# Kernel tuning notes

Hardware: AMD Instinct MI355X
Metric: run time of the kernel (lower is better)

The kernel has to match this reference:

```python
import jax, jax.numpy as jnp
import numpy as np

EMB = 1024
NHEAD = 16
HEAD_DIM = EMB // NHEAD  # 64
L = 2048
NEG = -1e30


def setup_inputs() -> dict:
    key = jax.random.key(0)
    ks = jax.random.split(key, 8)
    # xavier_uniform bound for square [EMB, EMB] matrices
    bound = float(np.sqrt(6.0 / (EMB + EMB)))
    def xavier(k):
        return jax.random.uniform(k, (EMB, EMB), jnp.float32, -bound, bound)
    return {
        "q": jax.random.normal(ks[0], (L, EMB), jnp.float32),
        "k": jax.random.normal(ks[1], (L, EMB), jnp.float32),
        "v": jax.random.normal(ks[2], (L, EMB), jnp.float32),
        "mask": jax.random.randint(ks[3], (NHEAD, L, L), 0, 2) > 0,
        "Wq": xavier(ks[4]),
        "Wk": xavier(ks[5]),
        "Wv": xavier(ks[6]),
        "Wo": xavier(ks[7]),
    }


def reference(q, k, v, mask, Wq, Wk, Wv, Wo):
    scaling = HEAD_DIM ** -0.5
    # F.linear(x, W) = x @ W.T ; reshape to [H, L, D]
    Q = (q @ Wq.T).reshape(L, NHEAD, HEAD_DIM).swapaxes(0, 1)
    K = (k @ Wk.T).reshape(L, NHEAD, HEAD_DIM).swapaxes(0, 1)
    V = (v @ Wv.T).reshape(L, NHEAD, HEAD_DIM).swapaxes(0, 1)
    scores = jnp.einsum("hld,hmd->hlm", Q, K) * scaling  # [H, L, L]
    scores = jnp.where(mask, jnp.asarray(NEG, scores.dtype), scores)
    p = jax.nn.softmax(scores, axis=-1)
    # attn_mask=True: multiplicative re-mask after softmax (custom path)
    p = p * (~mask).astype(p.dtype)
    # dropout is a no-op in eval mode
    attn_out = jnp.einsum("hlm,hmd->hld", p, V)  # [H, L, D]
    attn_out = attn_out.swapaxes(0, 1).reshape(L, EMB)
    return attn_out @ Wo.T
```

## Files before the change

### kernel.cpp

```cpp
#include <hip/hip_runtime.h>
#include <stdint.h>

#define EMB   1024
#define NHEAD 16
#define HDIM  64
#define SEQ   2048

typedef unsigned short ushort_t;
typedef unsigned int   uint32;
typedef __attribute__((ext_vector_type(8))) short bfrag;
typedef __attribute__((ext_vector_type(4))) float ffrag;

#define MFMA(a, b, c) __builtin_amdgcn_mfma_f32_16x16x32_bf16((a), (b), (c), 0, 0, 0)

__device__ inline ushort_t f2bf(float f) {
  uint32 u = __float_as_uint(f);
  u += 0x7FFFu + ((u >> 16) & 1u);
  return (ushort_t)(u >> 16);
}
__device__ inline uint32 pack2(float a, float b) {
  return (uint32)f2bf(a) | ((uint32)f2bf(b) << 16);
}

__device__ inline void glds16(const ushort_t* g, ushort_t* l) {
  __builtin_amdgcn_global_load_lds(
      (const __attribute__((address_space(1))) uint32*)(uintptr_t)g,
      (__attribute__((address_space(3))) uint32*)(uintptr_t)l, 16, 0, 0);
}

__global__ void detect_mask_kernel(const uint32* __restrict__ mw, int* __restrict__ flag) {
  uint32 w = mw[threadIdx.x];
  bool is4 = (w == 0u) || (w == 1u) || (w == 0x3F800000u);
  unsigned long long bad = __ballot(!is4);
  if (threadIdx.x == 0) flag[0] = (bad == 0ull) ? 1 : 0;
}

__global__ __launch_bounds__(256) void compress_mask(
    const void* __restrict__ maskp, const int* __restrict__ flag, ushort_t* __restrict__ bm)
{
  size_t t = (size_t)blockIdx.x * 256 + threadIdx.x;
  size_t row = t >> 7;
  int c16 = (int)(t & 127);
  size_t base = row * SEQ + (size_t)c16 * 16;
  ushort_t mv = 0;
  if (*flag) {
    const uint4* p = (const uint4*)((const uint32*)maskp + base);
    uint4 a0 = p[0], a1 = p[1], a2 = p[2], a3 = p[3];
    uint32 aw[16] = {a0.x,a0.y,a0.z,a0.w, a1.x,a1.y,a1.z,a1.w,
                     a2.x,a2.y,a2.z,a2.w, a3.x,a3.y,a3.z,a3.w};
    #pragma unroll
    for (int i = 0; i < 16; ++i) mv |= (ushort_t)((aw[i] != 0u) ? 1u : 0u) << i;
  } else {
    uint4 b0 = *(const uint4*)((const unsigned char*)maskp + base);
    uint32 bw[4] = {b0.x, b0.y, b0.z, b0.w};
    #pragma unroll
    for (int i = 0; i < 16; ++i)
      mv |= (ushort_t)((((bw[i >> 2] >> ((i & 3) * 8)) & 0xFFu) != 0u) ? 1u : 0u) << i;
  }
  bm[t] = mv;
}

__global__ __launch_bounds__(256) void cvt_all(
    const float4* __restrict__ q,  const float4* __restrict__ k,  const float4* __restrict__ v,
    const float4* __restrict__ wq, const float4* __restrict__ wk, const float4* __restrict__ wv,
    const float4* __restrict__ wo,
    uint2* __restrict__ qb,  uint2* __restrict__ kb,  uint2* __restrict__ vb,
    uint2* __restrict__ wqb, uint2* __restrict__ wkb, uint2* __restrict__ wvb,
    uint2* __restrict__ wob)
{
  int t = blockIdx.x * 256 + threadIdx.x;
  int s = blockIdx.y;
  const float4* src; uint2* dst; int n4;
  switch (s) {
    case 0: src = q;  dst = qb;  n4 = (SEQ * EMB) / 4; break;
    case 1: src = k;  dst = kb;  n4 = (SEQ * EMB) / 4; break;
    case 2: src = v;  dst = vb;  n4 = (SEQ * EMB) / 4; break;
    case 3: src = wq; dst = wqb; n4 = (EMB * EMB) / 4; break;
    case 4: src = wk; dst = wkb; n4 = (EMB * EMB) / 4; break;
    case 5: src = wv; dst = wvb; n4 = (EMB * EMB) / 4; break;
    default: src = wo; dst = wob; n4 = (EMB * EMB) / 4; break;
  }
  if (t >= n4) return;
  float4 f = src[t];
  uint2 o; o.x = pack2(f.x, f.y); o.y = pack2(f.z, f.w);
  dst[t] = o;
}

template<int MODE, int BN>
__device__ inline void gemm_body(const ushort_t* A, const ushort_t* B, void* Cp,
                                 int m0, int n0, ushort_t* As, ushort_t* Bs) {
  const int tid = threadIdx.x, lane = tid & 63, w = tid >> 6;
  const int wm = (w >> 1) * 64, wn = (w & 1) * (BN / 2);
  const int col = lane & 15, g = lane >> 4;
  constexpr int TN = BN / 32;
  constexpr int BIT = BN / 32;

  ffrag acc[4][TN] = {};

  for (int k0 = 0; k0 < EMB; k0 += 64) {
    __syncthreads();
    #pragma unroll
    for (int it = 0; it < 4; ++it) {
      int p = it * 256 + tid;
      int row = p >> 3, pc = p & 7;
      glds16(A + (size_t)(m0 + row) * EMB + k0 + (pc ^ (row & 7)) * 8, &As[p * 8]);
    }
    #pragma unroll
    for (int it = 0; it < BIT; ++it) {
      int p = it * 256 + tid;
      int row = p >> 3, pc = p & 7;
      glds16(B + (size_t)(n0 + row) * EMB + k0 + (pc ^ (row & 7)) * 8, &Bs[p * 8]);
    }
    __syncthreads();

    #pragma unroll
    for (int c = 0; c < 2; ++c) {
      bfrag av[4], bv[TN];
      #pragma unroll
      for (int t = 0; t < 4; ++t) {
        int ra = wm + t * 16 + col;
        av[t] = *(const bfrag*)&As[ra * 64 + ((c * 4 + g) ^ (ra & 7)) * 8];
      }
      #pragma unroll
      for (int t = 0; t < TN; ++t) {
        int rb = wn + t * 16 + col;
        bv[t] = *(const bfrag*)&Bs[rb * 64 + ((c * 4 + g) ^ (rb & 7)) * 8];
      }
      #pragma unroll
      for (int tm = 0; tm < 4; ++tm)
        #pragma unroll
        for (int tn = 0; tn < TN; ++tn)
          acc[tm][tn] = MFMA(av[tm], bv[tn], acc[tm][tn]);
    }
  }

  const int rbase = g * 4;
  #pragma unroll
  for (int tm = 0; tm < 4; ++tm)
    #pragma unroll
    for (int tn = 0; tn < TN; ++tn)
      #pragma unroll
      for (int r = 0; r < 4; ++r) {
        int m = m0 + wm + tm * 16 + rbase + r;
        int n = n0 + wn + tn * 16 + col;
        float vv = acc[tm][tn][r];
        if (MODE == 0) {
          ((ushort_t*)Cp)[((size_t)(n >> 6) * SEQ + m) * HDIM + (n & 63)] = f2bf(vv);
        } else if (MODE == 1) {
          ((ushort_t*)Cp)[((size_t)(m >> 6) * HDIM + (m & 63)) * SEQ + n] = f2bf(vv);
        } else {
          ((float*)Cp)[(size_t)m * EMB + n] = vv;
        }
      }
}

__global__ __launch_bounds__(256) void gemm_qkv(
    const ushort_t* __restrict__ qb, const ushort_t* __restrict__ kb, const ushort_t* __restrict__ vb,
    const ushort_t* __restrict__ Wqb, const ushort_t* __restrict__ Wkb, const ushort_t* __restrict__ Wvb,
    ushort_t* __restrict__ Qb, ushort_t* __restrict__ Kb, ushort_t* __restrict__ Vtb)
{
  __shared__ ushort_t As[128 * 64];
  __shared__ ushort_t Bs[64 * 64];
  const int z = blockIdx.y, bid = blockIdx.x;
  if (z == 0) {
    gemm_body<0, 64>(qb, Wqb, Qb, (bid >> 4) * 128, (bid & 15) * 64, As, Bs);
  } else if (z == 1) {
    gemm_body<0, 64>(kb, Wkb, Kb, (bid >> 4) * 128, (bid & 15) * 64, As, Bs);
  } else {
    gemm_body<1, 64>(Wvb, vb, Vtb, (bid >> 5) * 128, (bid & 31) * 64, As, Bs);
  }
}

__global__ __launch_bounds__(256) void gemm_out(
    const ushort_t* __restrict__ A, const ushort_t* __restrict__ B, float* __restrict__ C)
{
  __shared__ ushort_t As[128 * 64];
  __shared__ ushort_t Bs[64 * 64];
  gemm_body<2, 64>(A, B, (void*)C, blockIdx.y * 128, blockIdx.x * 64, As, Bs);
}

__global__ __launch_bounds__(256) void attn_mfma(
    const ushort_t* __restrict__ Qb,
    const ushort_t* __restrict__ Kb,
    const ushort_t* __restrict__ Vtb,
    const ushort_t* __restrict__ bm,
    ushort_t* __restrict__ attnb)
{
  __shared__ ushort_t KVs[2][2][64 * 64];
  __shared__ ushort_t Ps[4][16 * 72];

  const int tid  = threadIdx.x;
  const int lane = tid & 63;
  const int w    = tid >> 6;
  const int h    = blockIdx.y;
  const int l0   = blockIdx.x * 64;
  const int col  = lane & 15, g = lane >> 4, kg8 = g * 8, rbase = g * 4;

  ushort_t* pw = &Ps[w][0];

  {
    int rl = lane >> 2, seg = (lane & 3) * 16;
    const uint4* pq = (const uint4*)(Qb + ((size_t)h * SEQ + l0 + w * 16 + rl) * HDIM + seg);
    uint4 q0 = pq[0], q1 = pq[1];
    *(uint4*)&pw[rl * 72 + seg] = q0;
    *(uint4*)&pw[rl * 72 + seg + 8] = q1;
  }
  bfrag qf[2];
  qf[0] = *(const bfrag*)&pw[col * 72 + kg8];
  qf[1] = *(const bfrag*)&pw[col * 72 + 32 + kg8];

  auto stage_kv = [&](int kt_, int buf) {
    #pragma unroll
    for (int it = 0; it < 2; ++it) {
      int p = it * 256 + tid;
      int row = p >> 3, pc = p & 7;
      int sc = (pc ^ (row & 7)) * 8;
      glds16(Kb + ((size_t)h * SEQ + kt_ + row) * HDIM + sc, &KVs[buf][0][p * 8]);
      glds16(Vtb + ((size_t)h * HDIM + row) * SEQ + kt_ + sc, &KVs[buf][1][p * 8]);
    }
  };
  stage_kv(0, 0);

  const size_t bmbase = ((size_t)h * SEQ + l0 + w * 16 + (lane >> 2)) * 128 + (lane & 3);
  ushort_t mv_next = bm[bmbase];

  float lsum[4] = {0.f, 0.f, 0.f, 0.f};
  ffrag oacc[4] = {};

  for (int t = 0; t < 32; ++t) {
    const int buf = t & 1;
    __syncthreads();
    stage_kv(((t + 1) & 31) * 64, buf ^ 1);

    const ushort_t* Kc = &KVs[buf][0][0];
    const ushort_t* Vc = &KVs[buf][1][0];

    ushort_t mv = mv_next;
    mv_next = bm[bmbase + ((t + 1) & 31) * 4];

    ffrag s[4] = {};
    #pragma unroll
    for (int c = 0; c < 2; ++c)
      #pragma unroll
      for (int tn = 0; tn < 4; ++tn) {
        int row = tn * 16 + col;
        bfrag kf = *(const bfrag*)&Kc[row * 64 + ((c * 4 + g) ^ (row & 7)) * 8];
        s[tn] = MFMA(qf[c], kf, s[tn]);
      }

    #pragma unroll
    for (int r = 0; r < 4; ++r) {
      #pragma unroll
      for (int tn = 0; tn < 4; ++tn) {
        int m16 = __shfl((int)mv, (rbase + r) * 4 + tn, 64);
        bool msk = ((m16 >> col) & 1) != 0;
        float x = s[tn][r] * 0.125f;
        float p = msk ? 0.f : __expf(x);
        lsum[r] += p;
        pw[(rbase + r) * 72 + tn * 16 + col] = f2bf(p);
      }
    }

    #pragma unroll
    for (int c = 0; c < 2; ++c) {
      bfrag af = *(const bfrag*)&pw[col * 72 + c * 32 + kg8];
      #pragma unroll
      for (int tn = 0; tn < 4; ++tn) {
        int row = tn * 16 + col;
        bfrag vf = *(const bfrag*)&Vc[row * 64 + ((c * 4 + g) ^ (row & 7)) * 8];
        oacc[tn] = MFMA(af, vf, oacc[tn]);
      }
    }
  }

  float inv[4];
  #pragma unroll
  for (int r = 0; r < 4; ++r) {
    float s_ = lsum[r];
    #pragma unroll
    for (int off = 1; off < 16; off <<= 1) s_ += __shfl_xor(s_, off, 64);
    inv[r] = (s_ > 0.f) ? (1.0f / s_) : 0.0f;
  }
  #pragma unroll
  for (int tn = 0; tn < 4; ++tn)
    #pragma unroll
    for (int r = 0; r < 4; ++r) {
      int qg = l0 + w * 16 + rbase + r;
      attnb[(size_t)qg * EMB + h * HDIM + tn * 16 + col] = f2bf(oacc[tn][r] * inv[r]);
    }
}

extern "C" void kernel_launch(void* const* d_in, const int* in_sizes, int n_in,
                              void* d_out, int out_size, void* d_ws, size_t ws_size,
                              hipStream_t stream) {
  const float* q    = (const float*)d_in[0];
  const float* k    = (const float*)d_in[1];
  const float* v    = (const float*)d_in[2];
  const void*  mask =               d_in[3];
  const float* Wq   = (const float*)d_in[4];
  const float* Wk   = (const float*)d_in[5];
  const float* Wv   = (const float*)d_in[6];
  const float* Wo   = (const float*)d_in[7];

  char* ws = (char*)d_ws;
  const size_t MB = 1024 * 1024;
  ushort_t* qb    = (ushort_t*)(ws);
  ushort_t* kb    = (ushort_t*)(ws + 4  * MB);
  ushort_t* vb    = (ushort_t*)(ws + 8  * MB);
  ushort_t* Wqb   = (ushort_t*)(ws + 12 * MB);
  ushort_t* Wkb   = (ushort_t*)(ws + 14 * MB);
  ushort_t* Wvb   = (ushort_t*)(ws + 16 * MB);
  ushort_t* Wob   = (ushort_t*)(ws + 18 * MB);
  ushort_t* Qb    = (ushort_t*)(ws + 20 * MB);
  ushort_t* Kb    = (ushort_t*)(ws + 24 * MB);
  ushort_t* Vtb   = (ushort_t*)(ws + 28 * MB);
  int*      flag  = (int*)     (ws + 32 * MB);
  ushort_t* bmask = (ushort_t*)(ws + 33 * MB);
  ushort_t* attnb = qb;

  detect_mask_kernel<<<1, 64, 0, stream>>>((const uint32*)mask, flag);

  compress_mask<<<16384, 256, 0, stream>>>(mask, flag, bmask);

  cvt_all<<<dim3((SEQ * EMB / 4 + 255) / 256, 7), 256, 0, stream>>>(
      (const float4*)q, (const float4*)k, (const float4*)v,
      (const float4*)Wq, (const float4*)Wk, (const float4*)Wv, (const float4*)Wo,
      (uint2*)qb, (uint2*)kb, (uint2*)vb,
      (uint2*)Wqb, (uint2*)Wkb, (uint2*)Wvb, (uint2*)Wob);

  gemm_qkv<<<dim3(256, 3), 256, 0, stream>>>(qb, kb, vb, Wqb, Wkb, Wvb, Qb, Kb, Vtb);

  attn_mfma<<<dim3(SEQ / 64, NHEAD), 256, 0, stream>>>(Qb, Kb, Vtb, bmask, attnb);

  gemm_out<<<dim3(16, 16), 256, 0, stream>>>(attnb, Wob, (float*)d_out);
}
```

Before: 482.3 us.

## Fuse prep kernels, widen GEMM tiles, transpose score MFMA for packed P writes

Merges the mask compression and fp32-to-bf16 conversion kernels into one prep launch, removing a launch and its tail. Doubles the GEMM N tile to 128 for the QKV and output projections, halving the grid while raising per-block reuse. In attention, the score MFMA operands are swapped so each lane holds four consecutive keys for one query. This allows packed 8-byte stores of P, a single running row sum, and a shorter final reduction. Risks include lower occupancy or too few blocks from the larger tiles and changed LDS bank patterns.

```diff
diff --git a/kernel.cpp b/kernel.cpp
--- a/kernel.cpp
+++ b/kernel.cpp
@@ -35,32 +35,8 @@
   if (threadIdx.x == 0) flag[0] = (bad == 0ull) ? 1 : 0;
 }
 
-__global__ __launch_bounds__(256) void compress_mask(
-    const void* __restrict__ maskp, const int* __restrict__ flag, ushort_t* __restrict__ bm)
-{
-  size_t t = (size_t)blockIdx.x * 256 + threadIdx.x;
-  size_t row = t >> 7;
-  int c16 = (int)(t & 127);
-  size_t base = row * SEQ + (size_t)c16 * 16;
-  ushort_t mv = 0;
-  if (*flag) {
-    const uint4* p = (const uint4*)((const uint32*)maskp + base);
-    uint4 a0 = p[0], a1 = p[1], a2 = p[2], a3 = p[3];
-    uint32 aw[16] = {a0.x,a0.y,a0.z,a0.w, a1.x,a1.y,a1.z,a1.w,
-                     a2.x,a2.y,a2.z,a2.w, a3.x,a3.y,a3.z,a3.w};
-    #pragma unroll
-    for (int i = 0; i < 16; ++i) mv |= (ushort_t)((aw[i] != 0u) ? 1u : 0u) << i;
-  } else {
-    uint4 b0 = *(const uint4*)((const unsigned char*)maskp + base);
-    uint32 bw[4] = {b0.x, b0.y, b0.z, b0.w};
-    #pragma unroll
-    for (int i = 0; i < 16; ++i)
-      mv |= (ushort_t)((((bw[i >> 2] >> ((i & 3) * 8)) & 0xFFu) != 0u) ? 1u : 0u) << i;
-  }
-  bm[t] = mv;
-}
-
-__global__ __launch_bounds__(256) void cvt_all(
+__global__ __launch_bounds__(256) void prep(
+    const void* __restrict__ maskp, const int* __restrict__ flag, ushort_t* __restrict__ bmout,
     const float4* __restrict__ q,  const float4* __restrict__ k,  const float4* __restrict__ v,
     const float4* __restrict__ wq, const float4* __restrict__ wk, const float4* __restrict__ wv,
     const float4* __restrict__ wo,
@@ -68,19 +44,42 @@
     uint2* __restrict__ wqb, uint2* __restrict__ wkb, uint2* __restrict__ wvb,
     uint2* __restrict__ wob)
 {
-  int t = blockIdx.x * 256 + threadIdx.x;
-  int s = blockIdx.y;
-  const float4* src; uint2* dst; int n4;
-  switch (s) {
-    case 0: src = q;  dst = qb;  n4 = (SEQ * EMB) / 4; break;
-    case 1: src = k;  dst = kb;  n4 = (SEQ * EMB) / 4; break;
-    case 2: src = v;  dst = vb;  n4 = (SEQ * EMB) / 4; break;
-    case 3: src = wq; dst = wqb; n4 = (EMB * EMB) / 4; break;
-    case 4: src = wk; dst = wkb; n4 = (EMB * EMB) / 4; break;
-    case 5: src = wv; dst = wvb; n4 = (EMB * EMB) / 4; break;
-    default: src = wo; dst = wob; n4 = (EMB * EMB) / 4; break;
-  }
-  if (t >= n4) return;
+  const int tid = threadIdx.x;
+  int b = blockIdx.x;
+  if (b < 16384) {
+    size_t t = (size_t)b * 256 + tid;
+    size_t row = t >> 7;
+    int c16 = (int)(t & 127);
+    size_t base = row * SEQ + (size_t)c16 * 16;
+    ushort_t mv = 0;
+    if (*flag) {
+      const uint4* p = (const uint4*)((const uint32*)maskp + base);
+      uint4 a0 = p[0], a1 = p[1], a2 = p[2], a3 = p[3];
+      uint32 aw[16] = {a0.x,a0.y,a0.z,a0.w, a1.x,a1.y,a1.z,a1.w,
+                       a2.x,a2.y,a2.z,a2.w, a3.x,a3.y,a3.z,a3.w};
+      #pragma unroll
+      for (int i = 0; i < 16; ++i) mv |= (ushort_t)((aw[i] != 0u) ? 1u : 0u) << i;
+    } else {
+      uint4 b0 = *(const uint4*)((const unsigned char*)maskp + base);
+      uint32 bw[4] = {b0.x, b0.y, b0.z, b0.w};
+      #pragma unroll
+      for (int i = 0; i < 16; ++i)
+        mv |= (ushort_t)((((bw[i >> 2] >> ((i & 3) * 8)) & 0xFFu) != 0u) ? 1u : 0u) << i;
+    }
+    bmout[t] = mv;
+    return;
+  }
+  b -= 16384;
+  const float4* src; uint2* dst; int t;
+  if (b < 6144) {
+    int s = b >> 11; t = (b & 2047) * 256 + tid;
+    src = (s == 0) ? q  : (s == 1) ? k  : v;
+    dst = (s == 0) ? qb : (s == 1) ? kb : vb;
+  } else {
+    int s = (b - 6144) >> 10; t = ((b - 6144) & 1023) * 256 + tid;
+    src = (s == 0) ? wq  : (s == 1) ? wk  : (s == 2) ? wv  : wo;
+    dst = (s == 0) ? wqb : (s == 1) ? wkb : (s == 2) ? wvb : wob;
+  }
   float4 f = src[t];
   uint2 o; o.x = pack2(f.x, f.y); o.y = pack2(f.z, f.w);
   dst[t] = o;
@@ -160,14 +159,14 @@
     ushort_t* __restrict__ Qb, ushort_t* __restrict__ Kb, ushort_t* __restrict__ Vtb)
 {
   __shared__ ushort_t As[128 * 64];
-  __shared__ ushort_t Bs[64 * 64];
+  __shared__ ushort_t Bs[128 * 64];
   const int z = blockIdx.y, bid = blockIdx.x;
   if (z == 0) {
-    gemm_body<0, 64>(qb, Wqb, Qb, (bid >> 4) * 128, (bid & 15) * 64, As, Bs);
+    gemm_body<0, 128>(qb, Wqb, Qb, (bid >> 3) * 128, (bid & 7) * 128, As, Bs);
   } else if (z == 1) {
-    gemm_body<0, 64>(kb, Wkb, Kb, (bid >> 4) * 128, (bid & 15) * 64, As, Bs);
+    gemm_body<0, 128>(kb, Wkb, Kb, (bid >> 3) * 128, (bid & 7) * 128, As, Bs);
   } else {
-    gemm_body<1, 64>(Wvb, vb, Vtb, (bid >> 5) * 128, (bid & 31) * 64, As, Bs);
+    gemm_body<1, 128>(Wvb, vb, Vtb, (bid >> 4) * 128, (bid & 15) * 128, As, Bs);
   }
 }
 
@@ -175,8 +174,8 @@
     const ushort_t* __restrict__ A, const ushort_t* __restrict__ B, float* __restrict__ C)
 {
   __shared__ ushort_t As[128 * 64];
-  __shared__ ushort_t Bs[64 * 64];
-  gemm_body<2, 64>(A, B, (void*)C, blockIdx.y * 128, blockIdx.x * 64, As, Bs);
+  __shared__ ushort_t Bs[128 * 64];
+  gemm_body<2, 128>(A, B, (void*)C, blockIdx.y * 128, blockIdx.x * 128, As, Bs);
 }
 
 __global__ __launch_bounds__(256) void attn_mfma(
@@ -221,10 +220,10 @@
   };
   stage_kv(0, 0);
 
-  const size_t bmbase = ((size_t)h * SEQ + l0 + w * 16 + (lane >> 2)) * 128 + (lane & 3);
+  const size_t bmbase = ((size_t)h * SEQ + l0 + w * 16 + col) * 128 + g;
   ushort_t mv_next = bm[bmbase];
 
-  float lsum[4] = {0.f, 0.f, 0.f, 0.f};
+  float lsum = 0.f;
   ffrag oacc[4] = {};
 
   for (int t = 0; t < 32; ++t) {
@@ -235,8 +234,8 @@
     const ushort_t* Kc = &KVs[buf][0][0];
     const ushort_t* Vc = &KVs[buf][1][0];
 
-    ushort_t mv = mv_next;
-    mv_next = bm[bmbase + ((t + 1) & 31) * 4];
+    int mvi = (int)mv_next;
+    mv_next = bm[bmbase + (size_t)((t + 1) & 31) * 4];
 
     ffrag s[4] = {};
     #pragma unroll
@@ -245,20 +244,26 @@
       for (int tn = 0; tn < 4; ++tn) {
         int row = tn * 16 + col;
         bfrag kf = *(const bfrag*)&Kc[row * 64 + ((c * 4 + g) ^ (row & 7)) * 8];
-        s[tn] = MFMA(qf[c], kf, s[tn]);
-      }
-
-    #pragma unroll
-    for (int r = 0; r < 4; ++r) {
-      #pragma unroll
-      for (int tn = 0; tn < 4; ++tn) {
-        int m16 = __shfl((int)mv, (rbase + r) * 4 + tn, 64);
-        bool msk = ((m16 >> col) & 1) != 0;
-        float x = s[tn][r] * 0.125f;
-        float p = msk ? 0.f : __expf(x);
-        lsum[r] += p;
-        pw[(rbase + r) * 72 + tn * 16 + col] = f2bf(p);
-      }
+        s[tn] = MFMA(kf, qf[c], s[tn]);
+      }
+
+    #pragma unroll
+    for (int tn = 0; tn < 4; ++tn) {
+      int m16 = __shfl(mvi, tn * 16 + col, 64);
+      float p0, p1, p2, p3;
+      {
+        bool k0m = ((m16 >> (rbase + 0)) & 1) != 0;
+        bool k1m = ((m16 >> (rbase + 1)) & 1) != 0;
+        bool k2m = ((m16 >> (rbase + 2)) & 1) != 0;
+        bool k3m = ((m16 >> (rbase + 3)) & 1) != 0;
+        p0 = k0m ? 0.f : __expf(s[tn][0] * 0.125f);
+        p1 = k1m ? 0.f : __expf(s[tn][1] * 0.125f);
+        p2 = k2m ? 0.f : __expf(s[tn][2] * 0.125f);
+        p3 = k3m ? 0.f : __expf(s[tn][3] * 0.125f);
+      }
+      lsum += (p0 + p1) + (p2 + p3);
+      uint2 pk; pk.x = pack2(p0, p1); pk.y = pack2(p2, p3);
+      *(uint2*)&pw[col * 72 + tn * 16 + rbase] = pk;
     }
 
     #pragma unroll
@@ -273,14 +278,14 @@
     }
   }
 
+  float s_ = lsum;
+  s_ += __shfl_xor(s_, 16, 64);
+  s_ += __shfl_xor(s_, 32, 64);
+  float invf = (s_ > 0.f) ? (1.0f / s_) : 0.0f;
   float inv[4];
   #pragma unroll
-  for (int r = 0; r < 4; ++r) {
-    float s_ = lsum[r];
-    #pragma unroll
-    for (int off = 1; off < 16; off <<= 1) s_ += __shfl_xor(s_, off, 64);
-    inv[r] = (s_ > 0.f) ? (1.0f / s_) : 0.0f;
-  }
+  for (int r = 0; r < 4; ++r) inv[r] = __shfl(invf, rbase + r, 64);
+
   #pragma unroll
   for (int tn = 0; tn < 4; ++tn)
     #pragma unroll
@@ -320,17 +325,16 @@
 
   detect_mask_kernel<<<1, 64, 0, stream>>>((const uint32*)mask, flag);
 
-  compress_mask<<<16384, 256, 0, stream>>>(mask, flag, bmask);
-
-  cvt_all<<<dim3((SEQ * EMB / 4 + 255) / 256, 7), 256, 0, stream>>>(
+  prep<<<26624, 256, 0, stream>>>(
+      mask, flag, bmask,
       (const float4*)q, (const float4*)k, (const float4*)v,
       (const float4*)Wq, (const float4*)Wk, (const float4*)Wv, (const float4*)Wo,
       (uint2*)qb, (uint2*)kb, (uint2*)vb,
       (uint2*)Wqb, (uint2*)Wkb, (uint2*)Wvb, (uint2*)Wob);
 
-  gemm_qkv<<<dim3(256, 3), 256, 0, stream>>>(qb, kb, vb, Wqb, Wkb, Wvb, Qb, Kb, Vtb);
+  gemm_qkv<<<dim3(128, 3), 256, 0, stream>>>(qb, kb, vb, Wqb, Wkb, Wvb, Qb, Kb, Vtb);
 
   attn_mfma<<<dim3(SEQ / 64, NHEAD), 256, 0, stream>>>(Qb, Kb, Vtb, bmask, attnb);
 
-  gemm_out<<<dim3(16, 16), 256, 0, stream>>>(attnb, Wob, (float*)d_out);
-}
+  gemm_out<<<dim3(8, 16), 256, 0, stream>>>(attnb, Wob, (float*)d_out);
+}
```

Result: slower. 499.5 us (+3.6%).
